# Kernel tuning notes

Hardware: AMD Instinct MI355X
Metric: run time of the kernel (lower is better)

The kernel has to match this reference:

```python
import jax, jax.numpy as jnp
import numpy as np

N, J, P = 512, 20000, 8   # samples, genes (rna_count), covariates
DIM = J - 1               # pivot=True drops one column from the softmax logits


def setup_inputs() -> dict:
    key = jax.random.key(0)
    k0, k1, k2, k3, k4 = jax.random.split(key, 5)
    X = jax.random.normal(k0, (N, P), dtype=jnp.float32)
    # counts: non-negative integers stored as float (matches torch float64 Y of counts)
    Y = jnp.round(jax.random.uniform(k1, (N, J), dtype=jnp.float32) * 1000.0)
    mu = jax.random.normal(k2, (DIM,), dtype=jnp.float32)
    beta = jax.random.normal(k3, (P * DIM,), dtype=jnp.float32) * 0.1
    phi = jax.random.normal(k4, (J,), dtype=jnp.float32)
    return {"mu": mu, "beta": beta, "phi": phi, "X": X, "Y": Y}


def _nb_loglik(y, mean, disp):
    # NB with mean `mean` and dispersion `disp` (var = mean + disp*mean^2):
    # r = 1/disp, p = r/(r+mean)
    # log pmf = lgamma(y+r) - lgamma(r) - lgamma(y+1) + r*log(p) + y*log(1-p)
    r = 1.0 / disp
    log_rpm = jnp.log(r + mean)
    return (jax.lax.lgamma(y + r) - jax.lax.lgamma(r) - jax.lax.lgamma(y + 1.0)
            + r * (jnp.log(r) - log_rpm)
            + y * (jnp.log(mean) - log_rpm))


def reference(mu, beta, phi, X, Y):
    n, p = X.shape
    dim = mu.shape[0]
    beta_ = beta.reshape(p, dim)
    logits = mu + X @ beta_                                   # [N, J-1]
    logits = jnp.concatenate(
        [logits, jnp.zeros((n, 1), dtype=logits.dtype)], axis=1)  # pivot column of zeros -> [N, J]
    pi = jax.nn.softmax(logits, axis=1)                       # exp(logits - logsumexp)
    s = jnp.sum(Y, axis=1, keepdims=True)                     # [N, 1] total counts per sample
    mean = s * pi                                             # [N, J]
    disp = jax.nn.softplus(phi)                               # [J]
    log_lik = jnp.sum(_nb_loglik(Y, mean, disp))
    return log_lik.reshape(1)
```

## Files before the change

### kernel.cpp

```cpp
#include <hip/hip_runtime.h>

constexpr int N_SAMPLES = 512;
constexpr int J_GENES   = 20000;
constexpr int P_COV     = 8;
constexpr int DIM       = J_GENES - 1;
constexpr int BLOCK     = 256;
constexpr int TABLE_N   = 1024;

constexpr int CHUNK_G   = 1024;
constexpr int G_CHUNKS  = (J_GENES + CHUNK_G - 1) / CHUNK_G;
constexpr int ROWS      = 8;
constexpr int RGROUPS   = N_SAMPLES / ROWS;

constexpr size_t WS_RW    = 0;
constexpr size_t WS_KW    = WS_RW + J_GENES;
constexpr size_t WS_PS    = WS_KW + J_GENES;
constexpr size_t WS_PE    = WS_PS + (size_t)N_SAMPLES * G_CHUNKS;
constexpr size_t WS_TOTAL = WS_PE + (size_t)N_SAMPLES * G_CHUNKS;

__device__ inline float wave_reduce_sum(float v) {
#pragma unroll
    for (int off = 32; off > 0; off >>= 1)
        v += __shfl_down(v, off, 64);
    return v;
}

__device__ inline float lgamma_pos(float z) {
    float corr = 0.0f;
    if (z < 2.0f) {
        corr = -__logf(z * (z + 1.0f));
        z += 2.0f;
    }
    float lz  = __logf(z);
    float rz  = __builtin_amdgcn_rcpf(z);
    float rz2 = rz * rz;
    float ser = rz * fmaf(rz2, fmaf(rz2, 7.9365079365e-4f, -2.7777777778e-3f),
                          8.3333333333e-2f);
    return fmaf(z - 0.5f, lz, 0.91893853320467274f - z + ser + corr);
}

__device__ inline void load_gene_consts(const float* __restrict__ mu,
                                        const float* __restrict__ beta,
                                        int j0, bool valid,
                                        float muv[4], float bv[P_COV][4]) {
#pragma unroll
    for (int i = 0; i < 4; ++i) {
        const int j = j0 + i;
        const bool in = valid && (j < DIM);
        muv[i] = in ? mu[j] : 0.0f;
#pragma unroll
        for (int p = 0; p < P_COV; ++p)
            bv[p][i] = in ? beta[p * DIM + j] : 0.0f;
    }
}

__global__ __launch_bounds__(BLOCK) void phaseA_kernel(
    const float* __restrict__ mu, const float* __restrict__ beta,
    const float* __restrict__ phi, const float* __restrict__ X,
    const float* __restrict__ Y, float* __restrict__ ws,
    float* __restrict__ out) {
    const int t  = threadIdx.x;
    const int bx = blockIdx.x, by = blockIdx.y;
    const int j0 = bx * CHUNK_G + t * 4;
    const bool valid = j0 < J_GENES;

    if (by == 0) {
        if (bx == 0 && t == 0) out[0] = 0.0f;
        if (valid) {
#pragma unroll
            for (int i = 0; i < 4; ++i) {
                const int j = j0 + i;
                float ph = phi[j];
                float sp = (ph > 20.0f) ? ph : log1pf(__expf(ph));
                float r  = 1.0f / sp;
                float lr = -__logf(sp);
                ws[WS_RW + j] = r;
                ws[WS_KW + j] = fmaf(r, lr, -lgamma_pos(r));
            }
        }
    }

    float muv[4], bv[P_COV][4];
    load_gene_consts(mu, beta, j0, valid, muv, bv);

    __shared__ float redS[2][4], redE[2][4];
    const int n0 = by * ROWS;

    for (int rr = 0; rr < ROWS; ++rr) {
        const int n = n0 + rr;
        float x[P_COV];
#pragma unroll
        for (int p = 0; p < P_COV; ++p) x[p] = X[n * P_COV + p];

        float sa = 0.0f, ea = 0.0f;
        if (valid) {
            float4 y4 = *(const float4*)(Y + (size_t)n * J_GENES + j0);
            float lg[4];
#pragma unroll
            for (int i = 0; i < 4; ++i) {
                float v = muv[i];
#pragma unroll
                for (int p = 0; p < P_COV; ++p) v = fmaf(x[p], bv[p][i], v);
                lg[i] = v;
            }
            sa = (y4.x + y4.y) + (y4.z + y4.w);
            ea = (__expf(lg[0]) + __expf(lg[1])) + (__expf(lg[2]) + __expf(lg[3]));
        }

        float vs = wave_reduce_sum(sa);
        float ve = wave_reduce_sum(ea);
        const int b = rr & 1;
        if ((t & 63) == 0) { redS[b][t >> 6] = vs; redE[b][t >> 6] = ve; }
        __syncthreads();
        if (t == 0) {
            ws[WS_PS + (size_t)n * G_CHUNKS + bx] =
                (redS[b][0] + redS[b][1]) + (redS[b][2] + redS[b][3]);
            ws[WS_PE + (size_t)n * G_CHUNKS + bx] =
                (redE[b][0] + redE[b][1]) + (redE[b][2] + redE[b][3]);
        }
    }
}

__device__ inline float nb_elem(float y, float lg, float r, float K,
                                float c, float logc,
                                const float* __restrict__ tbl) {
    float mean = c * __expf(lg);
    float z    = y + r;
    float lrm  = __logf(r + mean);
    int   yi   = (int)(y + 0.5f);
    float lgy1 = (yi < TABLE_N) ? tbl[yi] : lgamma_pos(y + 1.0f);
    return (lgamma_pos(z) - lgy1 + K) + fmaf(-z, lrm, y * (logc + lg));
}

__global__ __launch_bounds__(BLOCK) void phaseB_kernel(
    const float* __restrict__ mu, const float* __restrict__ beta,
    const float* __restrict__ X, const float* __restrict__ Y,
    const float* __restrict__ ws_c, float* __restrict__ out) {
    const int t  = threadIdx.x;
    const int bx = blockIdx.x, by = blockIdx.y;
    const int j0 = bx * CHUNK_G + t * 4;
    const bool valid = j0 < J_GENES;
    const int n0 = by * ROWS;

    __shared__ __align__(16) float tbl[TABLE_N];
    __shared__ float shS[ROWS], shE[ROWS], shc[ROWS], shlc[ROWS];

#pragma unroll
    for (int i = 0; i < 4; ++i) {
        const int k = t * 4 + i;
        tbl[k] = (k < 2) ? 0.0f : lgamma_pos((float)k + 1.0f);
    }
    if (t < 2 * ROWS) {
        const int r = t & (ROWS - 1);
        const int which = t >> 3;
        const float* src = ws_c + (which ? WS_PE : WS_PS)
                         + (size_t)(n0 + r) * G_CHUNKS;
        float a = 0.0f;
#pragma unroll
        for (int k = 0; k < G_CHUNKS; ++k) a += src[k];
        if (which) shE[r] = a; else shS[r] = a;
    }
    __syncthreads();
    if (t < ROWS) {
        float c = shS[t] / shE[t];
        shc[t]  = c;
        shlc[t] = __logf(c);
    }

    float muv[4], bv[P_COV][4];
    load_gene_consts(mu, beta, j0, valid, muv, bv);
    float4 r4 = make_float4(1.f, 1.f, 1.f, 1.f);
    float4 K4 = make_float4(0.f, 0.f, 0.f, 0.f);
    if (valid) {
        r4 = *(const float4*)(ws_c + WS_RW + j0);
        K4 = *(const float4*)(ws_c + WS_KW + j0);
    }
    __syncthreads();

    float acc = 0.0f;
    for (int rr = 0; rr < ROWS; ++rr) {
        const int n = n0 + rr;
        const float c = shc[rr], logc = shlc[rr];
        float x[P_COV];
#pragma unroll
        for (int p = 0; p < P_COV; ++p) x[p] = X[n * P_COV + p];

        if (valid) {
            float4 y4 = *(const float4*)(Y + (size_t)n * J_GENES + j0);
            float lg[4];
#pragma unroll
            for (int i = 0; i < 4; ++i) {
                float v = muv[i];
#pragma unroll
                for (int p = 0; p < P_COV; ++p) v = fmaf(x[p], bv[p][i], v);
                lg[i] = v;
            }
            acc += nb_elem(y4.x, lg[0], r4.x, K4.x, c, logc, tbl);
            acc += nb_elem(y4.y, lg[1], r4.y, K4.y, c, logc, tbl);
            acc += nb_elem(y4.z, lg[2], r4.z, K4.z, c, logc, tbl);
            acc += nb_elem(y4.w, lg[3], r4.w, K4.w, c, logc, tbl);
        }
    }

    float v = wave_reduce_sum(acc);
    __shared__ float red[4];
    if ((t & 63) == 0) red[t >> 6] = v;
    __syncthreads();
    if (t == 0)
        atomicAdd(out, (red[0] + red[1]) + (red[2] + red[3]));
}

__global__ __launch_bounds__(BLOCK) void nb_mono(
    const float* __restrict__ mu, const float* __restrict__ beta,
    const float* __restrict__ phi, const float* __restrict__ X,
    const float* __restrict__ Y, float* __restrict__ out) {
    const int n = blockIdx.x;
    const int t = threadIdx.x;
    __shared__ float red[4];
    __shared__ float sh_s, sh_lse, sh_logs;
    float x[P_COV];
#pragma unroll
    for (int p = 0; p < P_COV; ++p) x[p] = X[n * P_COV + p];
    const float* yrow = Y + (size_t)n * J_GENES;
    float s_acc = 0.0f, e_acc = 0.0f;
    for (int j = t; j < J_GENES; j += BLOCK) {
        float logit = 0.0f;
        if (j < DIM) {
            logit = mu[j];
#pragma unroll
            for (int p = 0; p < P_COV; ++p)
                logit = fmaf(x[p], beta[p * DIM + j], logit);
        }
        s_acc += yrow[j];
        e_acc += __expf(logit);
    }
    float v = wave_reduce_sum(s_acc);
    if ((t & 63) == 0) red[t >> 6] = v;
    __syncthreads();
    if (t == 0) { float st = red[0]+red[1]+red[2]+red[3]; sh_s = st; sh_logs = __logf(st); }
    __syncthreads();
    v = wave_reduce_sum(e_acc);
    if ((t & 63) == 0) red[t >> 6] = v;
    __syncthreads();
    if (t == 0) sh_lse = __logf(red[0]+red[1]+red[2]+red[3]);
    __syncthreads();
    const float s = sh_s, logs = sh_logs, lse = sh_lse;
    float acc = 0.0f;
    for (int j = t; j < J_GENES; j += BLOCK) {
        float logit = 0.0f;
        if (j < DIM) {
            logit = mu[j];
#pragma unroll
            for (int p = 0; p < P_COV; ++p)
                logit = fmaf(x[p], beta[p * DIM + j], logit);
        }
        float ph = phi[j];
        float sp = (ph > 20.0f) ? ph : log1pf(__expf(ph));
        float r  = 1.0f / sp;
        float y  = yrow[j];
        float lp = logit - lse;
        float mean = s * __expf(lp);
        float lrm  = __logf(r + mean);
        acc += lgamma_pos(y + r) - lgamma_pos(r) - lgamma_pos(y + 1.0f)
             + fmaf(r, -__logf(sp) - lrm, y * ((logs + lp) - lrm));
    }
    v = wave_reduce_sum(acc);
    if ((t & 63) == 0) red[t >> 6] = v;
    __syncthreads();
    if (t == 0) atomicAdd(out, (red[0]+red[1])+(red[2]+red[3]));
}

__global__ void zero_out_kernel(float* __restrict__ out) { out[0] = 0.0f; }

extern "C" void kernel_launch(void* const* d_in, const int* in_sizes, int n_in,
                              void* d_out, int out_size, void* d_ws, size_t ws_size,
                              hipStream_t stream) {
    const float* mu   = (const float*)d_in[0];
    const float* beta = (const float*)d_in[1];
    const float* phi  = (const float*)d_in[2];
    const float* X    = (const float*)d_in[3];
    const float* Y    = (const float*)d_in[4];
    float* out = (float*)d_out;
    float* ws  = (float*)d_ws;

    if (ws_size >= WS_TOTAL * sizeof(float)) {
        dim3 grid(G_CHUNKS, RGROUPS);
        phaseA_kernel<<<grid, BLOCK, 0, stream>>>(mu, beta, phi, X, Y, ws, out);
        phaseB_kernel<<<grid, BLOCK, 0, stream>>>(mu, beta, X, Y, ws, out);
    } else {
        zero_out_kernel<<<1, 1, 0, stream>>>(out);
        nb_mono<<<N_SAMPLES, BLOCK, 0, stream>>>(mu, beta, phi, X, Y, out);
    }
}
```

Measured before the change: 127.5 us.

## Fuse two phases into one cooperative kernel with a grid sync

Merges the row-sum/exp-sum pass and the log-likelihood pass into a single cooperative kernel that keeps mu/beta in registers and uses a grid-wide barrier between phases. The gene chunking changes to 16 chunks of 1280 genes, with 5 strided scalar loads per thread instead of one float4. Per-wave partials are written directly, which removes the block-level shared reduction in the first phase. This saves one launch and the reload of gene constants, but requires all 1024 blocks to be co-resident (launch bounds 4 per SM). If the cooperative launch fails, the slow monolithic fallback runs instead.

```diff
diff --git a/kernel.cpp b/kernel.cpp
--- a/kernel.cpp
+++ b/kernel.cpp
@@ -1,4 +1,7 @@
 #include <hip/hip_runtime.h>
+#include <hip/hip_cooperative_groups.h>
+
+namespace cg = cooperative_groups;
 
 constexpr int N_SAMPLES = 512;
 constexpr int J_GENES   = 20000;
@@ -7,16 +10,18 @@
 constexpr int BLOCK     = 256;
 constexpr int TABLE_N   = 1024;
 
-constexpr int CHUNK_G   = 1024;
-constexpr int G_CHUNKS  = (J_GENES + CHUNK_G - 1) / CHUNK_G;
+constexpr int G_CHUNKS  = 16;
+constexpr int CHUNK_G   = 1280;
+constexpr int GPT       = 5;
 constexpr int ROWS      = 8;
 constexpr int RGROUPS   = N_SAMPLES / ROWS;
+constexpr int WAVES     = BLOCK / 64;
 
 constexpr size_t WS_RW    = 0;
 constexpr size_t WS_KW    = WS_RW + J_GENES;
 constexpr size_t WS_PS    = WS_KW + J_GENES;
-constexpr size_t WS_PE    = WS_PS + (size_t)N_SAMPLES * G_CHUNKS;
-constexpr size_t WS_TOTAL = WS_PE + (size_t)N_SAMPLES * G_CHUNKS;
+constexpr size_t WS_PE    = WS_PS + (size_t)N_SAMPLES * G_CHUNKS * WAVES;
+constexpr size_t WS_TOTAL = WS_PE + (size_t)N_SAMPLES * G_CHUNKS * WAVES;
 
 __device__ inline float wave_reduce_sum(float v) {
 #pragma unroll
@@ -37,88 +42,6 @@
     float ser = rz * fmaf(rz2, fmaf(rz2, 7.9365079365e-4f, -2.7777777778e-3f),
                           8.3333333333e-2f);
     return fmaf(z - 0.5f, lz, 0.91893853320467274f - z + ser + corr);
-}
-
-__device__ inline void load_gene_consts(const float* __restrict__ mu,
-                                        const float* __restrict__ beta,
-                                        int j0, bool valid,
-                                        float muv[4], float bv[P_COV][4]) {
-#pragma unroll
-    for (int i = 0; i < 4; ++i) {
-        const int j = j0 + i;
-        const bool in = valid && (j < DIM);
-        muv[i] = in ? mu[j] : 0.0f;
-#pragma unroll
-        for (int p = 0; p < P_COV; ++p)
-            bv[p][i] = in ? beta[p * DIM + j] : 0.0f;
-    }
-}
-
-__global__ __launch_bounds__(BLOCK) void phaseA_kernel(
-    const float* __restrict__ mu, const float* __restrict__ beta,
-    const float* __restrict__ phi, const float* __restrict__ X,
-    const float* __restrict__ Y, float* __restrict__ ws,
-    float* __restrict__ out) {
-    const int t  = threadIdx.x;
-    const int bx = blockIdx.x, by = blockIdx.y;
-    const int j0 = bx * CHUNK_G + t * 4;
-    const bool valid = j0 < J_GENES;
-
-    if (by == 0) {
-        if (bx == 0 && t == 0) out[0] = 0.0f;
-        if (valid) {
-#pragma unroll
-            for (int i = 0; i < 4; ++i) {
-                const int j = j0 + i;
-                float ph = phi[j];
-                float sp = (ph > 20.0f) ? ph : log1pf(__expf(ph));
-                float r  = 1.0f / sp;
-                float lr = -__logf(sp);
-                ws[WS_RW + j] = r;
-                ws[WS_KW + j] = fmaf(r, lr, -lgamma_pos(r));
-            }
-        }
-    }
-
-    float muv[4], bv[P_COV][4];
-    load_gene_consts(mu, beta, j0, valid, muv, bv);
-
-    __shared__ float redS[2][4], redE[2][4];
-    const int n0 = by * ROWS;
-
-    for (int rr = 0; rr < ROWS; ++rr) {
-        const int n = n0 + rr;
-        float x[P_COV];
-#pragma unroll
-        for (int p = 0; p < P_COV; ++p) x[p] = X[n * P_COV + p];
-
-        float sa = 0.0f, ea = 0.0f;
-        if (valid) {
-            float4 y4 = *(const float4*)(Y + (size_t)n * J_GENES + j0);
-            float lg[4];
-#pragma unroll
-            for (int i = 0; i < 4; ++i) {
-                float v = muv[i];
-#pragma unroll
-                for (int p = 0; p < P_COV; ++p) v = fmaf(x[p], bv[p][i], v);
-                lg[i] = v;
-            }
-            sa = (y4.x + y4.y) + (y4.z + y4.w);
-            ea = (__expf(lg[0]) + __expf(lg[1])) + (__expf(lg[2]) + __expf(lg[3]));
-        }
-
-        float vs = wave_reduce_sum(sa);
-        float ve = wave_reduce_sum(ea);
-        const int b = rr & 1;
-        if ((t & 63) == 0) { redS[b][t >> 6] = vs; redE[b][t >> 6] = ve; }
-        __syncthreads();
-        if (t == 0) {
-            ws[WS_PS + (size_t)n * G_CHUNKS + bx] =
-                (redS[b][0] + redS[b][1]) + (redS[b][2] + redS[b][3]);
-            ws[WS_PE + (size_t)n * G_CHUNKS + bx] =
-                (redE[b][0] + redE[b][1]) + (redE[b][2] + redE[b][3]);
-        }
-    }
 }
 
 __device__ inline float nb_elem(float y, float lg, float r, float K,
@@ -132,48 +55,111 @@
     return (lgamma_pos(z) - lgy1 + K) + fmaf(-z, lrm, y * (logc + lg));
 }
 
-__global__ __launch_bounds__(BLOCK) void phaseB_kernel(
+__global__ __launch_bounds__(BLOCK, 4) void nb_coop(
     const float* __restrict__ mu, const float* __restrict__ beta,
-    const float* __restrict__ X, const float* __restrict__ Y,
-    const float* __restrict__ ws_c, float* __restrict__ out) {
-    const int t  = threadIdx.x;
-    const int bx = blockIdx.x, by = blockIdx.y;
-    const int j0 = bx * CHUNK_G + t * 4;
-    const bool valid = j0 < J_GENES;
-    const int n0 = by * ROWS;
+    const float* __restrict__ phi, const float* __restrict__ X,
+    const float* __restrict__ Y, float* __restrict__ ws,
+    float* __restrict__ out) {
+    const int t    = threadIdx.x;
+    const int bx   = blockIdx.x;
+    const int by   = blockIdx.y;
+    const int wave = t >> 6;
+    const int base = bx * CHUNK_G + t;
+    const int n0   = by * ROWS;
+
+    bool  gv[GPT];
+    float muv[GPT], bv[P_COV][GPT];
+#pragma unroll
+    for (int k = 0; k < GPT; ++k) {
+        const int j = base + 256 * k;
+        gv[k] = (j < J_GENES);
+        const bool bvld = (j < DIM);
+        muv[k] = bvld ? mu[j] : 0.0f;
+#pragma unroll
+        for (int p = 0; p < P_COV; ++p)
+            bv[p][k] = bvld ? beta[p * DIM + j] : 0.0f;
+    }
+
+    if (by == 0) {
+        if (bx == 0 && t == 0) out[0] = 0.0f;
+#pragma unroll
+        for (int k = 0; k < GPT; ++k) {
+            const int j = base + 256 * k;
+            if (j < J_GENES) {
+                float ph = phi[j];
+                float sp = (ph > 20.0f) ? ph : log1pf(__expf(ph));
+                float r  = 1.0f / sp;
+                float lr = -__logf(sp);
+                ws[WS_RW + j] = r;
+                ws[WS_KW + j] = fmaf(r, lr, -lgamma_pos(r));
+            }
+        }
+    }
+
+    for (int rr = 0; rr < ROWS; ++rr) {
+        const int n = n0 + rr;
+        float x[P_COV];
+#pragma unroll
+        for (int p = 0; p < P_COV; ++p) x[p] = X[n * P_COV + p];
+
+        float sa = 0.0f, ea = 0.0f;
+#pragma unroll
+        for (int k = 0; k < GPT; ++k) {
+            if (gv[k]) {
+                const int j = base + 256 * k;
+                float y  = Y[(size_t)n * J_GENES + j];
+                float lg = muv[k];
+#pragma unroll
+                for (int p = 0; p < P_COV; ++p) lg = fmaf(x[p], bv[p][k], lg);
+                sa += y;
+                ea += __expf(lg);
+            }
+        }
+        float vs = wave_reduce_sum(sa);
+        float ve = wave_reduce_sum(ea);
+        if ((t & 63) == 0) {
+            const size_t slot = ((size_t)n * G_CHUNKS + bx) * WAVES + wave;
+            ws[WS_PS + slot] = vs;
+            ws[WS_PE + slot] = ve;
+        }
+    }
+
+    __threadfence();
+    cg::this_grid().sync();
 
     __shared__ __align__(16) float tbl[TABLE_N];
-    __shared__ float shS[ROWS], shE[ROWS], shc[ROWS], shlc[ROWS];
+    __shared__ float shSE[2 * ROWS];
+    __shared__ float shc[ROWS], shlc[ROWS];
+    __shared__ float red[WAVES];
 
 #pragma unroll
     for (int i = 0; i < 4; ++i) {
-        const int k = t * 4 + i;
-        tbl[k] = (k < 2) ? 0.0f : lgamma_pos((float)k + 1.0f);
+        const int kk = t * 4 + i;
+        tbl[kk] = (kk < 2) ? 0.0f : lgamma_pos((float)kk + 1.0f);
     }
     if (t < 2 * ROWS) {
         const int r = t & (ROWS - 1);
         const int which = t >> 3;
-        const float* src = ws_c + (which ? WS_PE : WS_PS)
-                         + (size_t)(n0 + r) * G_CHUNKS;
+        const float* src = ws + (which ? WS_PE : WS_PS)
+                         + (size_t)(n0 + r) * G_CHUNKS * WAVES;
         float a = 0.0f;
 #pragma unroll
-        for (int k = 0; k < G_CHUNKS; ++k) a += src[k];
-        if (which) shE[r] = a; else shS[r] = a;
+        for (int q = 0; q < G_CHUNKS * WAVES; ++q) a += src[q];
+        shSE[t] = a;
     }
     __syncthreads();
     if (t < ROWS) {
-        float c = shS[t] / shE[t];
+        float c = shSE[t] / shSE[t + ROWS];
         shc[t]  = c;
         shlc[t] = __logf(c);
     }
 
-    float muv[4], bv[P_COV][4];
-    load_gene_consts(mu, beta, j0, valid, muv, bv);
-    float4 r4 = make_float4(1.f, 1.f, 1.f, 1.f);
-    float4 K4 = make_float4(0.f, 0.f, 0.f, 0.f);
-    if (valid) {
-        r4 = *(const float4*)(ws_c + WS_RW + j0);
-        K4 = *(const float4*)(ws_c + WS_KW + j0);
+    float rv[GPT], Kv[GPT];
+#pragma unroll
+    for (int k = 0; k < GPT; ++k) {
+        const int j = base + 256 * k;
+        rv[k] = gv[k] ? ws[WS_RW + j] : 1.0f;
+        Kv[k] = gv[k] ? ws[WS_KW + j] : 0.0f;
     }
     __syncthreads();
 
@@ -185,26 +171,21 @@
 #pragma unroll
         for (int p = 0; p < P_COV; ++p) x[p] = X[n * P_COV + p];
 
-        if (valid) {
-            float4 y4 = *(const float4*)(Y + (size_t)n * J_GENES + j0);
-            float lg[4];
-#pragma unroll
-            for (int i = 0; i < 4; ++i) {
-                float v = muv[i];
-#pragma unroll
-                for (int p = 0; p < P_COV; ++p) v = fmaf(x[p], bv[p][i], v);
-                lg[i] = v;
+#pragma unroll
+        for (int k = 0; k < GPT; ++k) {
+            if (gv[k]) {
+                const int j = base + 256 * k;
+                float y  = Y[(size_t)n * J_GENES + j];
+                float lg = muv[k];
+#pragma unroll
+                for (int p = 0; p < P_COV; ++p) lg = fmaf(x[p], bv[p][k], lg);
+                acc += nb_elem(y, lg, rv[k], Kv[k], c, logc, tbl);
             }
-            acc += nb_elem(y4.x, lg[0], r4.x, K4.x, c, logc, tbl);
-            acc += nb_elem(y4.y, lg[1], r4.y, K4.y, c, logc, tbl);
-            acc += nb_elem(y4.z, lg[2], r4.z, K4.z, c, logc, tbl);
-            acc += nb_elem(y4.w, lg[3], r4.w, K4.w, c, logc, tbl);
         }
     }
 
     float v = wave_reduce_sum(acc);
-    __shared__ float red[4];
-    if ((t & 63) == 0) red[t >> 6] = v;
+    if ((t & 63) == 0) red[wave] = v;
     __syncthreads();
     if (t == 0)
         atomicAdd(out, (red[0] + red[1]) + (red[2] + red[3]));
@@ -283,11 +264,16 @@
     float* out = (float*)d_out;
     float* ws  = (float*)d_ws;
 
+    bool done = false;
     if (ws_size >= WS_TOTAL * sizeof(float)) {
         dim3 grid(G_CHUNKS, RGROUPS);
-        phaseA_kernel<<<grid, BLOCK, 0, stream>>>(mu, beta, phi, X, Y, ws, out);
-        phaseB_kernel<<<grid, BLOCK, 0, stream>>>(mu, beta, X, Y, ws, out);
-    } else {
+        void* args[] = {(void*)&mu, (void*)&beta, (void*)&phi, (void*)&X,
+                        (void*)&Y,  (void*)&ws,   (void*)&out};
+        hipError_t err = hipLaunchCooperativeKernel(
+            (const void*)nb_coop, grid, dim3(BLOCK), args, 0, stream);
+        done = (err == hipSuccess);
+    }
+    if (!done) {
         zero_out_kernel<<<1, 1, 0, stream>>>(out);
         nb_mono<<<N_SAMPLES, BLOCK, 0, stream>>>(mu, beta, phi, X, Y, out);
     }
```

Result: slower. 292.6 us (+129.5%).
